# Kernel tuning notes

Measured on AMD Instinct MI355X. Metric: run time of the kernel, lower is better.

Reference implementation:

```python
import jax, jax.numpy as jnp
import numpy as np

NUM_HEADS = 12
DIM_HEADS = 8  # number of sub-heads the depth is split into


def _split_into_heads(x, num_heads, dim_heads):
    # x: [B, S, E] -> [B, H, D, S, sub]  (D = dim_heads, sub = E/(H*D))
    B, S, E = x.shape
    depth = E // num_heads
    sub = depth // dim_heads
    x = x.reshape(B, S, num_heads, dim_heads, sub)
    return x.transpose(0, 2, 3, 1, 4)  # [B, H, D, S, sub]


def setup_inputs() -> dict:
    key = jax.random.key(0)
    ks = jax.random.split(key, 8)
    B, S, E = 2, 1024, 768
    sc_in = 1.0 / np.sqrt(E)
    return {
        "k": jax.random.normal(ks[0], (B, S, E), dtype=jnp.float32),
        "q": jax.random.normal(ks[1], (B, S, E), dtype=jnp.float32),
        "Wq_w": jax.random.normal(ks[2], (E, E), dtype=jnp.float32) * sc_in,
        "Wq_b": jax.random.normal(ks[3], (E,), dtype=jnp.float32) * 0.01,
        "Wk_w": jax.random.normal(ks[4], (E, E), dtype=jnp.float32) * sc_in,
        "Wk_b": jax.random.normal(ks[5], (E,), dtype=jnp.float32) * 0.01,
        "lin_w": jax.random.normal(ks[6], (DIM_HEADS,), dtype=jnp.float32) * (1.0 / np.sqrt(DIM_HEADS)),
        "lin_b": jax.random.normal(ks[7], (), dtype=jnp.float32) * 0.01,
    }


def reference(k, q, Wq_w, Wq_b, Wk_w, Wk_b, lin_w, lin_b):
    # Linear projections (torch Linear: x @ W^T + b)
    qp = q @ Wq_w.T + Wq_b  # [B, S, E]
    kp = k @ Wk_w.T + Wk_b  # [B, S, E]

    qh = _split_into_heads(qp, NUM_HEADS, DIM_HEADS)  # [B, H, D, S, sub]
    kh = _split_into_heads(kp, NUM_HEADS, DIM_HEADS)  # [B, H, D, S, sub]
    sub = kh.shape[-1]
    scale = 1.0 / np.sqrt(sub).astype(np.float32)

    # Original: scores[b,h,d,i,j] = (qh @ kh^T)/sqrt(sub), permute to [b,h,i,j,d],
    # dropout (identity at eval), then Linear(D,1).squeeze(-1).
    out = jnp.einsum("bhdis,bhdjs,d->bhij", qh, kh, lin_w) * scale + lin_b
    return out  # [B, H, S, S]
```

## Files before the change

kernel.cpp:

```cpp
#include <hip/hip_runtime.h>
#include <hip/hip_bf16.h>

#define B_ 2
#define S_ 1024
#define E_ 768
#define H_ 12

typedef __bf16  bf16x8 __attribute__((ext_vector_type(8)));
typedef float   f32x4  __attribute__((ext_vector_type(4)));

__device__ __forceinline__ unsigned short f2bf(float f) {
    union { float f; unsigned u; } a; a.f = f;
    unsigned u = a.u;
    u += 0x7FFFu + ((u >> 16) & 1u);
    return (unsigned short)(u >> 16);
}

__global__ __launch_bounds__(256) void cast_in_kernel(
    const float* __restrict__ q, const float* __restrict__ k,
    unsigned short* __restrict__ qbf, unsigned short* __restrict__ kbf)
{
    const float* src = blockIdx.z ? k : q;
    unsigned short* dst = blockIdx.z ? kbf : qbf;
    int i = (blockIdx.x * 256 + threadIdx.x) * 4;
    float4 v = *(const float4*)(src + i);
    ushort4 o = make_ushort4(f2bf(v.x), f2bf(v.y), f2bf(v.z), f2bf(v.w));
    *(ushort4*)(dst + i) = o;
}

__global__ __launch_bounds__(256) void prep_w_kernel(
    const float* __restrict__ Wq, const float* __restrict__ bq,
    const float* __restrict__ Wk, const float* __restrict__ lin_w,
    unsigned short* __restrict__ Wqbf, unsigned short* __restrict__ Wkbf,
    float* __restrict__ bqs)
{
    const float invs = 0.35355339059327373f;
    int idx4 = blockIdx.x * 256 + threadIdx.x;
    int i = idx4 * 4;
    if (blockIdx.z == 0) {
        int n = i / E_;
        float w = lin_w[(n & 63) >> 3] * invs;
        float4 v = *(const float4*)(Wq + i);
        ushort4 o = make_ushort4(f2bf(v.x * w), f2bf(v.y * w), f2bf(v.z * w), f2bf(v.w * w));
        *(ushort4*)(Wqbf + i) = o;
        if (idx4 < E_) bqs[idx4] = bq[idx4] * (lin_w[(idx4 & 63) >> 3] * invs);
    } else {
        float4 v = *(const float4*)(Wk + i);
        ushort4 o = make_ushort4(f2bf(v.x), f2bf(v.y), f2bf(v.z), f2bf(v.w));
        *(ushort4*)(Wkbf + i) = o;
    }
}

__device__ __forceinline__ void stage_tile(const unsigned short* __restrict__ g,
                                           int ld, char* lbase, int tid)
{
#pragma unroll
    for (int pass = 0; pass < 4; ++pass) {
        int c = pass * 256 + tid;
        int row = c >> 3, cb = c & 7;
        int cbg = cb ^ (row & 7);
        const unsigned short* src = g + row * ld + cbg * 8;
        __builtin_amdgcn_global_load_lds(
            (const __attribute__((address_space(1))) void*)src,
            (__attribute__((address_space(3))) void*)(lbase + c * 16),
            16, 0, 0);
    }
}

__device__ __forceinline__ bf16x8 ld_frag(const char* lbase, int row, int kk, int lane) {
    int cbyte = (kk * 64 + ((lane >> 4) * 16)) ^ ((row & 7) << 4);
    return *(const bf16x8*)(lbase + row * 128 + cbyte);
}

__global__ __launch_bounds__(256) void proj_kernel(
    const unsigned short* __restrict__ qbf, const unsigned short* __restrict__ kbf,
    const unsigned short* __restrict__ Wqbf, const unsigned short* __restrict__ Wkbf,
    const float* __restrict__ bqs, const float* __restrict__ bk,
    unsigned short* __restrict__ qs, unsigned short* __restrict__ kp)
{
    __shared__ char lds[2 * 128 * 64 * 2];
    char* As = lds;
    char* Bs = lds + 128 * 64 * 2;

    const unsigned short* X = blockIdx.z ? kbf : qbf;
    const unsigned short* W = blockIdx.z ? Wkbf : Wqbf;
    const float* bias       = blockIdx.z ? bk : bqs;
    unsigned short* P       = blockIdx.z ? kp : qs;

    int tid = threadIdx.x, lane = tid & 63, wid = tid >> 6;
    int wr = wid >> 1, wc = wid & 1;
    int tm = blockIdx.y * 128, tn = blockIdx.x * 128;

    f32x4 acc[4][4];
#pragma unroll
    for (int n = 0; n < 4; ++n) {
        float bv = bias[tn + wc * 64 + n * 16 + (lane & 15)];
#pragma unroll
        for (int m = 0; m < 4; ++m) acc[m][n] = f32x4{bv, bv, bv, bv};
    }

    for (int kb = 0; kb < E_; kb += 64) {
        stage_tile(X + tm * E_ + kb, E_, As, tid);
        stage_tile(W + tn * E_ + kb, E_, Bs, tid);
        __syncthreads();
#pragma unroll
        for (int kk = 0; kk < 2; ++kk) {
            bf16x8 a[4], b[4];
#pragma unroll
            for (int m = 0; m < 4; ++m) a[m] = ld_frag(As, wr * 64 + m * 16 + (lane & 15), kk, lane);
#pragma unroll
            for (int n = 0; n < 4; ++n) b[n] = ld_frag(Bs, wc * 64 + n * 16 + (lane & 15), kk, lane);
#pragma unroll
            for (int m = 0; m < 4; ++m)
#pragma unroll
                for (int n = 0; n < 4; ++n)
                    acc[m][n] = __builtin_amdgcn_mfma_f32_16x16x32_bf16(a[m], b[n], acc[m][n], 0, 0, 0);
        }
        __syncthreads();
    }

#pragma unroll
    for (int m = 0; m < 4; ++m)
#pragma unroll
        for (int n = 0; n < 4; ++n) {
            int col = tn + wc * 64 + n * 16 + (lane & 15);
            int rbase = tm + wr * 64 + m * 16 + ((lane >> 4) << 2);
#pragma unroll
            for (int r = 0; r < 4; ++r)
                P[(rbase + r) * E_ + col] = f2bf(acc[m][n][r]);
        }
}

__global__ __launch_bounds__(256) void scores_kernel(
    const unsigned short* __restrict__ qs, const unsigned short* __restrict__ kp,
    const float* __restrict__ lin_b, float* __restrict__ out)
{
    __shared__ char lds[2 * 128 * 64 * 2];
    char* As = lds;
    char* Bs = lds + 128 * 64 * 2;

    int z = blockIdx.z;
    int b = z / H_, h = z - b * H_;
    int tid = threadIdx.x, lane = tid & 63, wid = tid >> 6;
    int wr = wid >> 1, wc = wid & 1;
    int ti = blockIdx.y * 128, tj = blockIdx.x * 128;

    const unsigned short* Q = qs + (size_t)(b * S_ + ti) * E_ + h * 64;
    const unsigned short* K = kp + (size_t)(b * S_ + tj) * E_ + h * 64;
    stage_tile(Q, E_, As, tid);
    stage_tile(K, E_, Bs, tid);

    float lb = lin_b[0];
    f32x4 acc[4][4];
#pragma unroll
    for (int m = 0; m < 4; ++m)
#pragma unroll
        for (int n = 0; n < 4; ++n) acc[m][n] = f32x4{lb, lb, lb, lb};

    __syncthreads();
#pragma unroll
    for (int kk = 0; kk < 2; ++kk) {
        bf16x8 a[4], bfr[4];
#pragma unroll
        for (int m = 0; m < 4; ++m) a[m] = ld_frag(As, wr * 64 + m * 16 + (lane & 15), kk, lane);
#pragma unroll
        for (int n = 0; n < 4; ++n) bfr[n] = ld_frag(Bs, wc * 64 + n * 16 + (lane & 15), kk, lane);
#pragma unroll
        for (int m = 0; m < 4; ++m)
#pragma unroll
            for (int n = 0; n < 4; ++n)
                acc[m][n] = __builtin_amdgcn_mfma_f32_16x16x32_bf16(a[m], bfr[n], acc[m][n], 0, 0, 0);
    }

    float* O = out + ((size_t)z << 20);
#pragma unroll
    for (int m = 0; m < 4; ++m)
#pragma unroll
        for (int n = 0; n < 4; ++n) {
            int col = tj + wc * 64 + n * 16 + (lane & 15);
            int rbase = ti + wr * 64 + m * 16 + ((lane >> 4) << 2);
#pragma unroll
            for (int r = 0; r < 4; ++r)
                O[(size_t)(rbase + r) * S_ + col] = acc[m][n][r];
        }
}

extern "C" void kernel_launch(void* const* d_in, const int* in_sizes, int n_in,
                              void* d_out, int out_size, void* d_ws, size_t ws_size,
                              hipStream_t stream)
{
    const float* k_in  = (const float*)d_in[0];
    const float* q_in  = (const float*)d_in[1];
    const float* Wq_w  = (const float*)d_in[2];
    const float* Wq_b  = (const float*)d_in[3];
    const float* Wk_w  = (const float*)d_in[4];
    const float* Wk_b  = (const float*)d_in[5];
    const float* lin_w = (const float*)d_in[6];
    const float* lin_b = (const float*)d_in[7];
    float* out = (float*)d_out;

    char* ws = (char*)d_ws;
    unsigned short* qbf  = (unsigned short*)(ws + 0);
    unsigned short* kbf  = (unsigned short*)(ws + 3145728);
    unsigned short* Wqbf = (unsigned short*)(ws + 6291456);
    unsigned short* Wkbf = (unsigned short*)(ws + 7471104);
    float*          bqs  = (float*)        (ws + 8650752);
    unsigned short* qsb  = (unsigned short*)(ws + 8653824);
    unsigned short* kpb  = (unsigned short*)(ws + 11799552);

    cast_in_kernel<<<dim3(1536, 1, 2), dim3(256), 0, stream>>>(q_in, k_in, qbf, kbf);
    prep_w_kernel<<<dim3(576, 1, 2), dim3(256), 0, stream>>>(Wq_w, Wq_b, Wk_w, lin_w, Wqbf, Wkbf, bqs);
    proj_kernel<<<dim3(6, 16, 2), dim3(256), 0, stream>>>(qbf, kbf, Wqbf, Wkbf, bqs, Wk_b, qsb, kpb);
    scores_kernel<<<dim3(8, 8, 24), dim3(256), 0, stream>>>(qsb, kpb, lin_b, out);
}
```

Before: 50.71 us.

## Fuse fp32-to-bf16 input cast into projection GEMM and shrink tiles to 64x64

Drops the separate cast kernel. The projection kernel now reads fp32 q/k straight from global memory, converts them to bf16 in registers and writes them into swizzled LDS. The projection tile shrinks from 128x128 to 64x64, giving 768 blocks instead of 192 to fill the GPU. This removes one launch and a bf16 round trip through memory, but the fp32 loads go through registers rather than async global_load_lds, the inputs are re-read by more column blocks, and each block reuses less data per tile.

New measurement: 49.72 us. About the same (-2.0%).

```diff
diff --git a/kernel.cpp b/kernel.cpp
--- a/kernel.cpp
+++ b/kernel.cpp
@@ -8,24 +8,13 @@
 
 typedef __bf16  bf16x8 __attribute__((ext_vector_type(8)));
 typedef float   f32x4  __attribute__((ext_vector_type(4)));
+typedef unsigned short u16x8 __attribute__((ext_vector_type(8)));
 
 __device__ __forceinline__ unsigned short f2bf(float f) {
     union { float f; unsigned u; } a; a.f = f;
     unsigned u = a.u;
     u += 0x7FFFu + ((u >> 16) & 1u);
     return (unsigned short)(u >> 16);
-}
-
-__global__ __launch_bounds__(256) void cast_in_kernel(
-    const float* __restrict__ q, const float* __restrict__ k,
-    unsigned short* __restrict__ qbf, unsigned short* __restrict__ kbf)
-{
-    const float* src = blockIdx.z ? k : q;
-    unsigned short* dst = blockIdx.z ? kbf : qbf;
-    int i = (blockIdx.x * 256 + threadIdx.x) * 4;
-    float4 v = *(const float4*)(src + i);
-    ushort4 o = make_ushort4(f2bf(v.x), f2bf(v.y), f2bf(v.z), f2bf(v.w));
-    *(ushort4*)(dst + i) = o;
 }
 
 __global__ __launch_bounds__(256) void prep_w_kernel(
@@ -51,7 +40,42 @@
     }
 }
 
-__device__ __forceinline__ void stage_tile(const unsigned short* __restrict__ g,
+
+__device__ __forceinline__ void stage_x64_f32(const float* __restrict__ g,
+                                              int ld, char* lbase, int tid)
+{
+#pragma unroll
+    for (int pass = 0; pass < 2; ++pass) {
+        int c = pass * 256 + tid;
+        int row = c >> 3, cb = c & 7;
+        int cbg = cb ^ (row & 7);
+        const float* src = g + row * ld + cbg * 8;
+        float4 v0 = *(const float4*)(src);
+        float4 v1 = *(const float4*)(src + 4);
+        u16x8 o;
+        o[0] = f2bf(v0.x); o[1] = f2bf(v0.y); o[2] = f2bf(v0.z); o[3] = f2bf(v0.w);
+        o[4] = f2bf(v1.x); o[5] = f2bf(v1.y); o[6] = f2bf(v1.z); o[7] = f2bf(v1.w);
+        *(u16x8*)(lbase + c * 16) = o;
+    }
+}
+
+__device__ __forceinline__ void stage_w64(const unsigned short* __restrict__ g,
+                                          int ld, char* lbase, int tid)
+{
+#pragma unroll
+    for (int pass = 0; pass < 2; ++pass) {
+        int c = pass * 256 + tid;
+        int row = c >> 3, cb = c & 7;
+        int cbg = cb ^ (row & 7);
+        const unsigned short* src = g + row * ld + cbg * 8;
+        __builtin_amdgcn_global_load_lds(
+            (const __attribute__((address_space(1))) void*)src,
+            (__attribute__((address_space(3))) void*)(lbase + c * 16),
+            16, 0, 0);
+    }
+}
+
+__device__ __forceinline__ void stage_w128(const unsigned short* __restrict__ g,
                                            int ld, char* lbase, int tid)
 {
 #pragma unroll
@@ -73,61 +97,61 @@
 }
 
 __global__ __launch_bounds__(256) void proj_kernel(
-    const unsigned short* __restrict__ qbf, const unsigned short* __restrict__ kbf,
+    const float* __restrict__ q_in, const float* __restrict__ k_in,
     const unsigned short* __restrict__ Wqbf, const unsigned short* __restrict__ Wkbf,
     const float* __restrict__ bqs, const float* __restrict__ bk,
     unsigned short* __restrict__ qs, unsigned short* __restrict__ kp)
 {
-    __shared__ char lds[2 * 128 * 64 * 2];
+    __shared__ char lds[2 * 64 * 64 * 2];
     char* As = lds;
-    char* Bs = lds + 128 * 64 * 2;
-
-    const unsigned short* X = blockIdx.z ? kbf : qbf;
+    char* Bs = lds + 64 * 64 * 2;
+
+    const float* X          = blockIdx.z ? k_in : q_in;
     const unsigned short* W = blockIdx.z ? Wkbf : Wqbf;
     const float* bias       = blockIdx.z ? bk : bqs;
     unsigned short* P       = blockIdx.z ? kp : qs;
 
     int tid = threadIdx.x, lane = tid & 63, wid = tid >> 6;
     int wr = wid >> 1, wc = wid & 1;
-    int tm = blockIdx.y * 128, tn = blockIdx.x * 128;
-
-    f32x4 acc[4][4];
-#pragma unroll
-    for (int n = 0; n < 4; ++n) {
-        float bv = bias[tn + wc * 64 + n * 16 + (lane & 15)];
-#pragma unroll
-        for (int m = 0; m < 4; ++m) acc[m][n] = f32x4{bv, bv, bv, bv};
+    int tm = blockIdx.y * 64, tn = blockIdx.x * 64;
+
+    f32x4 acc[2][2];
+#pragma unroll
+    for (int n = 0; n < 2; ++n) {
+        float bv = bias[tn + wc * 32 + n * 16 + (lane & 15)];
+#pragma unroll
+        for (int m = 0; m < 2; ++m) acc[m][n] = f32x4{bv, bv, bv, bv};
     }
 
     for (int kb = 0; kb < E_; kb += 64) {
-        stage_tile(X + tm * E_ + kb, E_, As, tid);
-        stage_tile(W + tn * E_ + kb, E_, Bs, tid);
+        stage_x64_f32(X + (size_t)tm * E_ + kb, E_, As, tid);
+        stage_w64(W + (size_t)tn * E_ + kb, E_, Bs, tid);
         __syncthreads();
 #pragma unroll
         for (int kk = 0; kk < 2; ++kk) {
-            bf16x8 a[4], b[4];
-#pragma unroll
-            for (int m = 0; m < 4; ++m) a[m] = ld_frag(As, wr * 64 + m * 16 + (lane & 15), kk, lane);
-#pragma unroll
-            for (int n = 0; n < 4; ++n) b[n] = ld_frag(Bs, wc * 64 + n * 16 + (lane & 15), kk, lane);
-#pragma unroll
-            for (int m = 0; m < 4; ++m)
-#pragma unroll
-                for (int n = 0; n < 4; ++n)
+            bf16x8 a[2], b[2];
+#pragma unroll
+            for (int m = 0; m < 2; ++m) a[m] = ld_frag(As, wr * 32 + m * 16 + (lane & 15), kk, lane);
+#pragma unroll
+            for (int n = 0; n < 2; ++n) b[n] = ld_frag(Bs, wc * 32 + n * 16 + (lane & 15), kk, lane);
+#pragma unroll
+            for (int m = 0; m < 2; ++m)
+#pragma unroll
+                for (int n = 0; n < 2; ++n)
                     acc[m][n] = __builtin_amdgcn_mfma_f32_16x16x32_bf16(a[m], b[n], acc[m][n], 0, 0, 0);
         }
         __syncthreads();
     }
 
 #pragma unroll
-    for (int m = 0; m < 4; ++m)
-#pragma unroll
-        for (int n = 0; n < 4; ++n) {
-            int col = tn + wc * 64 + n * 16 + (lane & 15);
-            int rbase = tm + wr * 64 + m * 16 + ((lane >> 4) << 2);
+    for (int m = 0; m < 2; ++m)
+#pragma unroll
+        for (int n = 0; n < 2; ++n) {
+            int col = tn + wc * 32 + n * 16 + (lane & 15);
+            int rbase = tm + wr * 32 + m * 16 + ((lane >> 4) << 2);
 #pragma unroll
             for (int r = 0; r < 4; ++r)
-                P[(rbase + r) * E_ + col] = f2bf(acc[m][n][r]);
+                P[(size_t)(rbase + r) * E_ + col] = f2bf(acc[m][n][r]);
         }
 }
 
@@ -147,8 +171,8 @@
 
     const unsigned short* Q = qs + (size_t)(b * S_ + ti) * E_ + h * 64;
     const unsigned short* K = kp + (size_t)(b * S_ + tj) * E_ + h * 64;
-    stage_tile(Q, E_, As, tid);
-    stage_tile(K, E_, Bs, tid);
+    stage_w128(Q, E_, As, tid);
+    stage_w128(K, E_, Bs, tid);
 
     float lb = lin_b[0];
     f32x4 acc[4][4];
@@ -200,16 +224,13 @@
     float* out = (float*)d_out;
 
     char* ws = (char*)d_ws;
-    unsigned short* qbf  = (unsigned short*)(ws + 0);
-    unsigned short* kbf  = (unsigned short*)(ws + 3145728);
-    unsigned short* Wqbf = (unsigned short*)(ws + 6291456);
-    unsigned short* Wkbf = (unsigned short*)(ws + 7471104);
-    float*          bqs  = (float*)        (ws + 8650752);
-    unsigned short* qsb  = (unsigned short*)(ws + 8653824);
-    unsigned short* kpb  = (unsigned short*)(ws + 11799552);
-
-    cast_in_kernel<<<dim3(1536, 1, 2), dim3(256), 0, stream>>>(q_in, k_in, qbf, kbf);
+    unsigned short* Wqbf = (unsigned short*)(ws + 0);
+    unsigned short* Wkbf = (unsigned short*)(ws + 1179648);
+    float*          bqs  = (float*)        (ws + 2359296);
+    unsigned short* qsb  = (unsigned short*)(ws + 2362368);
+    unsigned short* kpb  = (unsigned short*)(ws + 5508096);
+
     prep_w_kernel<<<dim3(576, 1, 2), dim3(256), 0, stream>>>(Wq_w, Wq_b, Wk_w, lin_w, Wqbf, Wkbf, bqs);
-    proj_kernel<<<dim3(6, 16, 2), dim3(256), 0, stream>>>(qbf, kbf, Wqbf, Wkbf, bqs, Wk_b, qsb, kpb);
+    proj_kernel<<<dim3(12, 32, 2), dim3(256), 0, stream>>>(q_in, k_in, Wqbf, Wkbf, bqs, Wk_b, qsb, kpb);
     scores_kernel<<<dim3(8, 8, 24), dim3(256), 0, stream>>>(qsb, kpb, lin_b, out);
 }
```

## Fuse fp32-to-bf16 casts into projection GEMM and retile both kernels

Applied to the files above, without the earlier changes.

Drops the separate cast kernels for the inputs and weights. The projection kernel now loads fp32 directly, converts to bf16 in registers, and writes to double-buffered LDS with a software-pipelined k-loop, using smaller 64x64 tiles to get more blocks. The scores kernel keeps Q fragments in registers, stages two 128-wide K tiles, and writes float4 vectorized outputs. This removes two launches and the extra global round trips through bf16 copies. In exchange, each projection block converts fp32 redundantly across tiles and does more global reads at fp32 width.

Measured after the change: 49.98 us. Within noise of the previous version (-1.4%).

```diff
diff --git a/kernel.cpp b/kernel.cpp
--- a/kernel.cpp
+++ b/kernel.cpp
@@ -1,13 +1,14 @@
 #include <hip/hip_runtime.h>
 #include <hip/hip_bf16.h>
 
-#define B_ 2
 #define S_ 1024
 #define E_ 768
 #define H_ 12
 
 typedef __bf16  bf16x8 __attribute__((ext_vector_type(8)));
 typedef float   f32x4  __attribute__((ext_vector_type(4)));
+typedef unsigned short u16x8 __attribute__((ext_vector_type(8)));
+typedef unsigned short u16x4 __attribute__((ext_vector_type(4)));
 
 __device__ __forceinline__ unsigned short f2bf(float f) {
     union { float f; unsigned u; } a; a.f = f;
@@ -16,55 +17,11 @@
     return (unsigned short)(u >> 16);
 }
 
-__global__ __launch_bounds__(256) void cast_in_kernel(
-    const float* __restrict__ q, const float* __restrict__ k,
-    unsigned short* __restrict__ qbf, unsigned short* __restrict__ kbf)
-{
-    const float* src = blockIdx.z ? k : q;
-    unsigned short* dst = blockIdx.z ? kbf : qbf;
-    int i = (blockIdx.x * 256 + threadIdx.x) * 4;
-    float4 v = *(const float4*)(src + i);
-    ushort4 o = make_ushort4(f2bf(v.x), f2bf(v.y), f2bf(v.z), f2bf(v.w));
-    *(ushort4*)(dst + i) = o;
-}
-
-__global__ __launch_bounds__(256) void prep_w_kernel(
-    const float* __restrict__ Wq, const float* __restrict__ bq,
-    const float* __restrict__ Wk, const float* __restrict__ lin_w,
-    unsigned short* __restrict__ Wqbf, unsigned short* __restrict__ Wkbf,
-    float* __restrict__ bqs)
-{
-    const float invs = 0.35355339059327373f;
-    int idx4 = blockIdx.x * 256 + threadIdx.x;
-    int i = idx4 * 4;
-    if (blockIdx.z == 0) {
-        int n = i / E_;
-        float w = lin_w[(n & 63) >> 3] * invs;
-        float4 v = *(const float4*)(Wq + i);
-        ushort4 o = make_ushort4(f2bf(v.x * w), f2bf(v.y * w), f2bf(v.z * w), f2bf(v.w * w));
-        *(ushort4*)(Wqbf + i) = o;
-        if (idx4 < E_) bqs[idx4] = bq[idx4] * (lin_w[(idx4 & 63) >> 3] * invs);
-    } else {
-        float4 v = *(const float4*)(Wk + i);
-        ushort4 o = make_ushort4(f2bf(v.x), f2bf(v.y), f2bf(v.z), f2bf(v.w));
-        *(ushort4*)(Wkbf + i) = o;
-    }
-}
-
-__device__ __forceinline__ void stage_tile(const unsigned short* __restrict__ g,
-                                           int ld, char* lbase, int tid)
-{
-#pragma unroll
-    for (int pass = 0; pass < 4; ++pass) {
-        int c = pass * 256 + tid;
-        int row = c >> 3, cb = c & 7;
-        int cbg = cb ^ (row & 7);
-        const unsigned short* src = g + row * ld + cbg * 8;
-        __builtin_amdgcn_global_load_lds(
-            (const __attribute__((address_space(1))) void*)src,
-            (__attribute__((address_space(3))) void*)(lbase + c * 16),
-            16, 0, 0);
-    }
+__device__ __forceinline__ u16x8 pack8(float4 a, float4 b, float w) {
+    u16x8 o;
+    o[0] = f2bf(a.x * w); o[1] = f2bf(a.y * w); o[2] = f2bf(a.z * w); o[3] = f2bf(a.w * w);
+    o[4] = f2bf(b.x * w); o[5] = f2bf(b.y * w); o[6] = f2bf(b.z * w); o[7] = f2bf(b.w * w);
+    return o;
 }
 
 __device__ __forceinline__ bf16x8 ld_frag(const char* lbase, int row, int kk, int lane) {
@@ -73,116 +30,175 @@
 }
 
 __global__ __launch_bounds__(256) void proj_kernel(
-    const unsigned short* __restrict__ qbf, const unsigned short* __restrict__ kbf,
-    const unsigned short* __restrict__ Wqbf, const unsigned short* __restrict__ Wkbf,
-    const float* __restrict__ bqs, const float* __restrict__ bk,
+    const float* __restrict__ q_in, const float* __restrict__ k_in,
+    const float* __restrict__ Wq, const float* __restrict__ Wk,
+    const float* __restrict__ bq, const float* __restrict__ bk,
+    const float* __restrict__ lin_w,
     unsigned short* __restrict__ qs, unsigned short* __restrict__ kp)
 {
-    __shared__ char lds[2 * 128 * 64 * 2];
-    char* As = lds;
-    char* Bs = lds + 128 * 64 * 2;
-
-    const unsigned short* X = blockIdx.z ? kbf : qbf;
-    const unsigned short* W = blockIdx.z ? Wkbf : Wqbf;
-    const float* bias       = blockIdx.z ? bk : bqs;
-    unsigned short* P       = blockIdx.z ? kp : qs;
+    __shared__ char lds[32768];
+
+    const float* X    = blockIdx.z ? k_in : q_in;
+    const float* W    = blockIdx.z ? Wk   : Wq;
+    const float* bias = blockIdx.z ? bk   : bq;
+    unsigned short* P = blockIdx.z ? kp   : qs;
+    const float invs = 0.35355339059327373f;
 
     int tid = threadIdx.x, lane = tid & 63, wid = tid >> 6;
-    int wr = wid >> 1, wc = wid & 1;
-    int tm = blockIdx.y * 128, tn = blockIdx.x * 128;
-
-    f32x4 acc[4][4];
-#pragma unroll
-    for (int n = 0; n < 4; ++n) {
-        float bv = bias[tn + wc * 64 + n * 16 + (lane & 15)];
-#pragma unroll
-        for (int m = 0; m < 4; ++m) acc[m][n] = f32x4{bv, bv, bv, bv};
+    int wn = wid >> 1, wm = wid & 1;
+    int tm = blockIdx.y * 64, tn = blockIdx.x * 64;
+
+    int c0 = tid,        r0 = c0 >> 3, g0 = ((c0 & 7) ^ (r0 & 7)) * 8;
+    int c1 = 256 + tid,  r1 = c1 >> 3, g1 = ((c1 & 7) ^ (r1 & 7)) * 8;
+    float sw0 = 1.0f, sw1 = 1.0f;
+    if (blockIdx.z == 0) { sw0 = lin_w[r0 >> 3] * invs; sw1 = lin_w[r1 >> 3] * invs; }
+
+    const float* Xg = X + (size_t)tm * E_;
+    const float* Wg = W + (size_t)tn * E_;
+
+    float4 xv0, xv1, xv2, xv3, wv0, wv1, wv2, wv3;
+#define LOADXW(kb) { \
+    const float* xs0 = Xg + r0 * E_ + (kb) + g0; xv0 = *(const float4*)xs0; xv1 = *(const float4*)(xs0 + 4); \
+    const float* xs1 = Xg + r1 * E_ + (kb) + g1; xv2 = *(const float4*)xs1; xv3 = *(const float4*)(xs1 + 4); \
+    const float* ws0 = Wg + r0 * E_ + (kb) + g0; wv0 = *(const float4*)ws0; wv1 = *(const float4*)(ws0 + 4); \
+    const float* ws1 = Wg + r1 * E_ + (kb) + g1; wv2 = *(const float4*)ws1; wv3 = *(const float4*)(ws1 + 4); }
+#define WRITEXW(buf) { \
+    char* xb = lds + (buf) * 8192; \
+    *(u16x8*)(xb + c0 * 16) = pack8(xv0, xv1, 1.0f); \
+    *(u16x8*)(xb + c1 * 16) = pack8(xv2, xv3, 1.0f); \
+    char* wb = lds + 16384 + (buf) * 8192; \
+    *(u16x8*)(wb + c0 * 16) = pack8(wv0, wv1, sw0); \
+    *(u16x8*)(wb + c1 * 16) = pack8(wv2, wv3, sw1); }
+
+    f32x4 acc[2][2];
+#pragma unroll
+    for (int nj = 0; nj < 2; ++nj) {
+        int n0 = tn + wn * 32 + nj * 16 + ((lane >> 4) << 2);
+        float4 b4 = *(const float4*)(bias + n0);
+        float w = (blockIdx.z == 0) ? lin_w[(n0 & 63) >> 3] * invs : 1.0f;
+#pragma unroll
+        for (int mi = 0; mi < 2; ++mi)
+            acc[nj][mi] = f32x4{b4.x * w, b4.y * w, b4.z * w, b4.w * w};
     }
 
-    for (int kb = 0; kb < E_; kb += 64) {
-        stage_tile(X + tm * E_ + kb, E_, As, tid);
-        stage_tile(W + tn * E_ + kb, E_, Bs, tid);
+#define COMPSTEP(buf) { \
+    const char* Xc = lds + (buf) * 8192; \
+    const char* Wc = lds + 16384 + (buf) * 8192; \
+    _Pragma("unroll") \
+    for (int kk = 0; kk < 2; ++kk) { \
+        bf16x8 a0 = ld_frag(Wc, wn * 32 + (lane & 15), kk, lane); \
+        bf16x8 a1 = ld_frag(Wc, wn * 32 + 16 + (lane & 15), kk, lane); \
+        bf16x8 b0 = ld_frag(Xc, wm * 32 + (lane & 15), kk, lane); \
+        bf16x8 b1 = ld_frag(Xc, wm * 32 + 16 + (lane & 15), kk, lane); \
+        acc[0][0] = __builtin_amdgcn_mfma_f32_16x16x32_bf16(a0, b0, acc[0][0], 0, 0, 0); \
+        acc[0][1] = __builtin_amdgcn_mfma_f32_16x16x32_bf16(a0, b1, acc[0][1], 0, 0, 0); \
+        acc[1][0] = __builtin_amdgcn_mfma_f32_16x16x32_bf16(a1, b0, acc[1][0], 0, 0, 0); \
+        acc[1][1] = __builtin_amdgcn_mfma_f32_16x16x32_bf16(a1, b1, acc[1][1], 0, 0, 0); \
+    } }
+
+    LOADXW(0);
+    WRITEXW(0);
+    __syncthreads();
+    int cur = 0;
+#pragma unroll 2
+    for (int t = 0; t < 11; ++t) {
+        LOADXW((t + 1) * 64);
+        COMPSTEP(cur);
+        WRITEXW(cur ^ 1);
         __syncthreads();
-#pragma unroll
-        for (int kk = 0; kk < 2; ++kk) {
-            bf16x8 a[4], b[4];
-#pragma unroll
-            for (int m = 0; m < 4; ++m) a[m] = ld_frag(As, wr * 64 + m * 16 + (lane & 15), kk, lane);
-#pragma unroll
-            for (int n = 0; n < 4; ++n) b[n] = ld_frag(Bs, wc * 64 + n * 16 + (lane & 15), kk, lane);
-#pragma unroll
-            for (int m = 0; m < 4; ++m)
-#pragma unroll
-                for (int n = 0; n < 4; ++n)
-                    acc[m][n] = __builtin_amdgcn_mfma_f32_16x16x32_bf16(a[m], b[n], acc[m][n], 0, 0, 0);
+        cur ^= 1;
+    }
+    COMPSTEP(cur);
+
+#pragma unroll
+    for (int nj = 0; nj < 2; ++nj)
+#pragma unroll
+        for (int mi = 0; mi < 2; ++mi) {
+            int n0 = tn + wn * 32 + nj * 16 + ((lane >> 4) << 2);
+            int m  = tm + wm * 32 + mi * 16 + (lane & 15);
+            u16x4 pk;
+            pk[0] = f2bf(acc[nj][mi][0]); pk[1] = f2bf(acc[nj][mi][1]);
+            pk[2] = f2bf(acc[nj][mi][2]); pk[3] = f2bf(acc[nj][mi][3]);
+            *(u16x4*)(P + (size_t)m * E_ + n0) = pk;
         }
-        __syncthreads();
-    }
-
-#pragma unroll
-    for (int m = 0; m < 4; ++m)
-#pragma unroll
-        for (int n = 0; n < 4; ++n) {
-            int col = tn + wc * 64 + n * 16 + (lane & 15);
-            int rbase = tm + wr * 64 + m * 16 + ((lane >> 4) << 2);
-#pragma unroll
-            for (int r = 0; r < 4; ++r)
-                P[(rbase + r) * E_ + col] = f2bf(acc[m][n][r]);
-        }
+#undef LOADXW
+#undef WRITEXW
+#undef COMPSTEP
 }
 
 __global__ __launch_bounds__(256) void scores_kernel(
     const unsigned short* __restrict__ qs, const unsigned short* __restrict__ kp,
     const float* __restrict__ lin_b, float* __restrict__ out)
 {
-    __shared__ char lds[2 * 128 * 64 * 2];
-    char* As = lds;
-    char* Bs = lds + 128 * 64 * 2;
-
-    int z = blockIdx.z;
-    int b = z / H_, h = z - b * H_;
+    __shared__ char lds[32768];
+
+    int z = blockIdx.z, b = z / H_, h = z - b * H_;
     int tid = threadIdx.x, lane = tid & 63, wid = tid >> 6;
-    int wr = wid >> 1, wc = wid & 1;
-    int ti = blockIdx.y * 128, tj = blockIdx.x * 128;
-
-    const unsigned short* Q = qs + (size_t)(b * S_ + ti) * E_ + h * 64;
-    const unsigned short* K = kp + (size_t)(b * S_ + tj) * E_ + h * 64;
-    stage_tile(Q, E_, As, tid);
-    stage_tile(K, E_, Bs, tid);
-
-    float lb = lin_b[0];
-    f32x4 acc[4][4];
-#pragma unroll
-    for (int m = 0; m < 4; ++m)
-#pragma unroll
-        for (int n = 0; n < 4; ++n) acc[m][n] = f32x4{lb, lb, lb, lb};
-
+    int wj = wid >> 1, wi = wid & 1;
+    int ti = blockIdx.y * 128, tj = blockIdx.x * 256;
+
+    const unsigned short* Qg = qs + (size_t)(b * S_) * E_ + h * 64;
+    const unsigned short* Kg = kp + (size_t)(b * S_) * E_ + h * 64;
+
+#define STAGEK(jbase, buf) { \
+    char* lb = lds + (buf) * 16384; \
+    _Pragma("unroll") \
+    for (int pass = 0; pass < 4; ++pass) { \
+        int c = pass * 256 + tid; \
+        int row = c >> 3, cbg = (c & 7) ^ (row & 7); \
+        __builtin_amdgcn_global_load_lds( \
+            (const __attribute__((address_space(1))) void*)(Kg + (size_t)((jbase) + row) * E_ + cbg * 8), \
+            (__attribute__((address_space(3))) void*)(lb + c * 16), 16, 0, 0); \
+    } }
+
+    bf16x8 qf[2][4];
+    int qrow = ti + wi * 64 + (lane & 15);
+#pragma unroll
+    for (int ni = 0; ni < 4; ++ni)
+#pragma unroll
+        for (int kk = 0; kk < 2; ++kk)
+            qf[kk][ni] = *(const bf16x8*)(Qg + (size_t)(qrow + ni * 16) * E_ + kk * 32 + ((lane >> 4) * 8));
+
+    float lb0 = lin_b[0];
+    float* O = out + ((size_t)z << 20);
+
+    STAGEK(tj, 0);
     __syncthreads();
-#pragma unroll
-    for (int kk = 0; kk < 2; ++kk) {
-        bf16x8 a[4], bfr[4];
-#pragma unroll
-        for (int m = 0; m < 4; ++m) a[m] = ld_frag(As, wr * 64 + m * 16 + (lane & 15), kk, lane);
-#pragma unroll
-        for (int n = 0; n < 4; ++n) bfr[n] = ld_frag(Bs, wc * 64 + n * 16 + (lane & 15), kk, lane);
-#pragma unroll
-        for (int m = 0; m < 4; ++m)
-#pragma unroll
-            for (int n = 0; n < 4; ++n)
-                acc[m][n] = __builtin_amdgcn_mfma_f32_16x16x32_bf16(a[m], bfr[n], acc[m][n], 0, 0, 0);
+    STAGEK(tj + 128, 1);
+
+#pragma unroll
+    for (int sub = 0; sub < 2; ++sub) {
+        f32x4 acc[4][4];
+#pragma unroll
+        for (int mj = 0; mj < 4; ++mj)
+#pragma unroll
+            for (int ni = 0; ni < 4; ++ni) acc[mj][ni] = f32x4{lb0, lb0, lb0, lb0};
+
+        const char* Kc = lds + sub * 16384;
+#pragma unroll
+        for (int kk = 0; kk < 2; ++kk) {
+            bf16x8 a[4];
+#pragma unroll
+            for (int mj = 0; mj < 4; ++mj) a[mj] = ld_frag(Kc, wj * 64 + mj * 16 + (lane & 15), kk, lane);
+#pragma unroll
+            for (int mj = 0; mj < 4; ++mj)
+#pragma unroll
+                for (int ni = 0; ni < 4; ++ni)
+                    acc[mj][ni] = __builtin_amdgcn_mfma_f32_16x16x32_bf16(a[mj], qf[kk][ni], acc[mj][ni], 0, 0, 0);
+        }
+
+#pragma unroll
+        for (int mj = 0; mj < 4; ++mj)
+#pragma unroll
+            for (int ni = 0; ni < 4; ++ni) {
+                int i  = ti + wi * 64 + ni * 16 + (lane & 15);
+                int j0 = tj + sub * 128 + wj * 64 + mj * 16 + ((lane >> 4) << 2);
+                *(float4*)(O + (size_t)i * S_ + j0) = (float4){acc[mj][ni][0], acc[mj][ni][1], acc[mj][ni][2], acc[mj][ni][3]};
+            }
+
+        if (sub == 0) __syncthreads();
     }
-
-    float* O = out + ((size_t)z << 20);
-#pragma unroll
-    for (int m = 0; m < 4; ++m)
-#pragma unroll
-        for (int n = 0; n < 4; ++n) {
-            int col = tj + wc * 64 + n * 16 + (lane & 15);
-            int rbase = ti + wr * 64 + m * 16 + ((lane >> 4) << 2);
-#pragma unroll
-            for (int r = 0; r < 4; ++r)
-                O[(size_t)(rbase + r) * S_ + col] = acc[m][n][r];
-        }
+#undef STAGEK
 }
 
 extern "C" void kernel_launch(void* const* d_in, const int* in_sizes, int n_in,
@@ -200,16 +216,9 @@
     float* out = (float*)d_out;
 
     char* ws = (char*)d_ws;
-    unsigned short* qbf  = (unsigned short*)(ws + 0);
-    unsigned short* kbf  = (unsigned short*)(ws + 3145728);
-    unsigned short* Wqbf = (unsigned short*)(ws + 6291456);
-    unsigned short* Wkbf = (unsigned short*)(ws + 7471104);
-    float*          bqs  = (float*)        (ws + 8650752);
-    unsigned short* qsb  = (unsigned short*)(ws + 8653824);
-    unsigned short* kpb  = (unsigned short*)(ws + 11799552);
-
-    cast_in_kernel<<<dim3(1536, 1, 2), dim3(256), 0, stream>>>(q_in, k_in, qbf, kbf);
-    prep_w_kernel<<<dim3(576, 1, 2), dim3(256), 0, stream>>>(Wq_w, Wq_b, Wk_w, lin_w, Wqbf, Wkbf, bqs);
-    proj_kernel<<<dim3(6, 16, 2), dim3(256), 0, stream>>>(qbf, kbf, Wqbf, Wkbf, bqs, Wk_b, qsb, kpb);
-    scores_kernel<<<dim3(8, 8, 24), dim3(256), 0, stream>>>(qsb, kpb, lin_b, out);
-}
+    unsigned short* qsb = (unsigned short*)(ws + 0);
+    unsigned short* kpb = (unsigned short*)(ws + 3145728);
+
+    proj_kernel<<<dim3(12, 32, 2), dim3(256), 0, stream>>>(q_in, k_in, Wq_w, Wk_w, Wq_b, Wk_b, lin_w, qsb, kpb);
+    scores_kernel<<<dim3(4, 8, 24), dim3(256), 0, stream>>>(qsb, kpb, lin_b, out);
+}
```
